# Kernel tuning notes

Hardware: AMD Instinct MI355X
Metric: run time of the kernel (lower is better)

The kernel has to match this reference:

```python
import jax, jax.numpy as jnp
import numpy as np

B, S, D = 1024, 200, 128
NQ, NC, NQD, NCD = 50000, 1000, 101, 101


def _linear_params(k, fan_in, fan_out):
    bound = 1.0 / np.sqrt(fan_in)
    kw, kb = jax.random.split(k)
    W = jax.random.uniform(kw, (fan_out, fan_in), minval=-bound, maxval=bound, dtype=jnp.float32)
    b = jax.random.uniform(kb, (fan_out,), minval=-bound, maxval=bound, dtype=jnp.float32)
    return W, b


def setup_inputs() -> dict:
    key = jax.random.key(0)
    ks = jax.random.split(key, 17)
    Wx, bx = _linear_params(ks[0], 4 * D, D)
    Ws1, bs1 = _linear_params(ks[1], D, D)
    Ws2, bs2 = _linear_params(ks[2], D, D)
    Wp1, bp1 = _linear_params(ks[3], 2 * D, D)
    Wp2, bp2 = _linear_params(ks[4], 2 * D, D)
    Wk, bk = _linear_params(ks[5], 4 * D, D)
    Eq = jax.random.normal(ks[6], (NQ, D), dtype=jnp.float32)
    Ec = jax.random.normal(ks[7], (NC, D), dtype=jnp.float32)
    Eqd = jax.random.normal(ks[8], (NQD, D), dtype=jnp.float32)
    Ecd = jax.random.normal(ks[9], (NCD, D), dtype=jnp.float32)
    Ecorr = jax.random.normal(ks[10], (2, D), dtype=jnp.float32)
    # xavier_uniform init for h_pre (torch: gain*sqrt(6/(fan_in+fan_out)) on [B,D])
    bh = np.sqrt(6.0 / (B + D))
    h0 = jax.random.uniform(ks[11], (B, D), minval=-bh, maxval=bh, dtype=jnp.float32)
    question_seq = jax.random.randint(ks[12], (B, S), 0, NQ)
    concept_seq = jax.random.randint(ks[13], (B, S), 0, NC)
    question_diff_seq = jax.random.randint(ks[14], (B, S), 0, NQD)
    concept_diff_seq = jax.random.randint(ks[15], (B, S), 0, NCD)
    correct_seq = jax.random.randint(ks[16], (B, S), 0, 2)
    return dict(question_seq=question_seq, concept_seq=concept_seq,
                question_diff_seq=question_diff_seq, concept_diff_seq=concept_diff_seq,
                correct_seq=correct_seq,
                Eq=Eq, Ec=Ec, Eqd=Eqd, Ecd=Ecd, Ecorr=Ecorr,
                Wx=Wx, bx=bx, Ws1=Ws1, bs1=bs1, Ws2=Ws2, bs2=bs2,
                Wp1=Wp1, bp1=bp1, Wp2=Wp2, bp2=bp2, Wk=Wk, bk=bk, h0=h0)


def reference(question_seq, concept_seq, question_diff_seq, concept_diff_seq, correct_seq,
              Eq, Ec, Eqd, Ecd, Ecorr,
              Wx, bx, Ws1, bs1, Ws2, bs2, Wp1, bp1, Wp2, bp2, Wk, bk, h0):
    qe = Eq[question_seq]            # [B,S,D]
    ce = Ec[concept_seq]
    qde = Eqd[question_diff_seq]
    cde = Ecd[concept_diff_seq]
    corr = Ecorr[correct_seq]
    # generate_x_MLP applied to all timesteps at once (same math as per-step)
    x = jnp.concatenate([qe, ce, qde, cde], axis=-1) @ Wx.T + bx  # [B,S,D]
    # time-major inputs for the scan over t = 0 .. S-2
    xs = (jnp.swapaxes(x[:, :-1], 0, 1),      # x_t       [S-1,B,D]
          jnp.swapaxes(x[:, 1:], 0, 1),       # x_{t+1}
          jnp.swapaxes(corr[:, :-1], 0, 1),
          jnp.swapaxes(qde[:, :-1], 0, 1),
          jnp.swapaxes(cde[:, :-1], 0, 1))

    def step(h_pre, inp):
        xt, xnext, ct, qdt, cdt = inp
        s_in = xt - h_pre
        sdf = jax.nn.sigmoid(s_in @ Ws1.T + bs1) * jnp.tanh(s_in @ Ws2.T + bs2)  # dropout=eval identity
        p_in = jnp.concatenate([sdf, ct], axis=-1)
        pka = jax.nn.sigmoid(p_in @ Wp1.T + bp1) * jnp.tanh(p_in @ Wp2.T + bp2)
        k_in = jnp.concatenate([h_pre, ct, qdt, cdt], axis=-1)
        g = jax.nn.sigmoid(k_in @ Wk.T + bk)
        h = g * h_pre + (1.0 - g) * pka
        yt = jax.nn.sigmoid(jnp.sum(xnext * h, axis=-1))  # [B]
        return h, yt

    _, ys = jax.lax.scan(step, h0, xs)  # ys: [S-1,B]
    y = jnp.concatenate([ys.T, jnp.zeros((question_seq.shape[0], 1), x.dtype)], axis=1)  # [B,S], y[:, S-1]=0
    return y
```

## Files before the change

### kernel.cpp

```cpp
#include <hip/hip_runtime.h>


#define S_LEN 200
#define NBATCH 1024
#define DIM 128
#define LOG2E 1.4426950408889634f

typedef short short8 __attribute__((ext_vector_type(8)));
typedef float f32x4 __attribute__((ext_vector_type(4)));

__device__ __forceinline__ unsigned short f2b(float f) {
  union { float f; unsigned u; } v; v.f = f;
  unsigned r = (v.u + 0x7FFFu + ((v.u >> 16) & 1u)) >> 16;
  return (unsigned short)r;
}
__device__ __forceinline__ float b2f(unsigned short b) {
  union { unsigned u; float f; } v; v.u = ((unsigned)b) << 16;
  return v.f;
}
__device__ __forceinline__ float fast_sigmoid(float x) {
  return __builtin_amdgcn_rcpf(1.0f + __builtin_amdgcn_exp2f(-LOG2E * x));
}
__device__ __forceinline__ float fast_tanh(float x) {
  return 2.0f * __builtin_amdgcn_rcpf(1.0f + __builtin_amdgcn_exp2f(-2.0f * LOG2E * x)) - 1.0f;
}
__device__ __forceinline__ void wg_barrier_lds() {
  __asm__ volatile("s_waitcnt lgkmcnt(0)\n\ts_barrier" ::: "memory");
}

__global__ void proj_all_kernel(const float* __restrict__ Eq, const float* __restrict__ Ec,
                                const float* __restrict__ Eqd, const float* __restrict__ Ecd,
                                const float* __restrict__ Ecorr,
                                const float* __restrict__ Wx,
                                const float* __restrict__ Wp1, const float* __restrict__ bp1,
                                const float* __restrict__ Wp2, const float* __restrict__ bp2,
                                const float* __restrict__ Wk, const float* __restrict__ bk,
                                unsigned short* __restrict__ Tq, unsigned short* __restrict__ Tc,
                                unsigned short* __restrict__ Tqd, unsigned short* __restrict__ Tcd,
                                unsigned short* __restrict__ Tkqd, unsigned short* __restrict__ Tkcd,
                                float* __restrict__ Tkc, float* __restrict__ Tp1c,
                                float* __restrict__ Tp2c) {
  const int bid = blockIdx.x;
  const int tid = threadIdx.x;
  if (bid >= 3202) {
    const int blk = bid - 3202;
    if (blk < 101) {
      const int o = tid & 127, half = tid >> 7;
      const float* e = (half ? Ecd : Eqd) + (size_t)blk * DIM;
      const float* wr = Wk + (size_t)o * 512 + (half ? 384 : 256);
      float a = 0.f;
      for (int k = 0; k < DIM; ++k) a = fmaf(e[k], wr[k], a);
      (half ? Tkcd : Tkqd)[blk * DIM + o] = f2b(a);
    } else {
      for (int idx = tid; idx < 768; idx += 256) {
        const int t = idx >> 8, e = (idx >> 7) & 1, o = idx & 127;
        const float* ec = Ecorr + e * DIM;
        const float* wr; float bias; float* dst;
        if (t == 0)      { wr = Wp1 + (size_t)o * 256 + 128; bias = bp1[o]; dst = Tp1c; }
        else if (t == 1) { wr = Wp2 + (size_t)o * 256 + 128; bias = bp2[o]; dst = Tp2c; }
        else             { wr = Wk  + (size_t)o * 512 + 128; bias = bk[o];  dst = Tkc;  }
        float a = bias;
        for (int k = 0; k < DIM; ++k) a = fmaf(ec[k], wr[k], a);
        dst[e * DIM + o] = a;
      }
    }
    return;
  }
  const float* E; int M, coff, r0; unsigned short* T;
  if (bid < 3125)      { E = Eq;  M = 50000; coff = 0;   T = Tq;  r0 = bid * 16; }
  else if (bid < 3188) { E = Ec;  M = 1000;  coff = 128; T = Tc;  r0 = (bid - 3125) * 16; }
  else if (bid < 3195) { E = Eqd; M = 101;   coff = 256; T = Tqd; r0 = (bid - 3188) * 16; }
  else                 { E = Ecd; M = 101;   coff = 384; T = Tcd; r0 = (bid - 3195) * 16; }

  __shared__ __align__(16) unsigned short A[16][136];
  {
    const int row = tid >> 4, c8 = (tid & 15) * 8;
    union U8 { uint4 v; unsigned short s[8]; } o;
    if (r0 + row < M) {
      const float4 e0 = *(const float4*)(E + (size_t)(r0 + row) * DIM + c8);
      const float4 e1 = *(const float4*)(E + (size_t)(r0 + row) * DIM + c8 + 4);
      o.s[0] = f2b(e0.x); o.s[1] = f2b(e0.y); o.s[2] = f2b(e0.z); o.s[3] = f2b(e0.w);
      o.s[4] = f2b(e1.x); o.s[5] = f2b(e1.y); o.s[6] = f2b(e1.z); o.s[7] = f2b(e1.w);
    } else {
      o.v = make_uint4(0, 0, 0, 0);
    }
    *(uint4*)&A[row][c8] = o.v;
  }
  __syncthreads();
  const int w = tid >> 6, L = tid & 63, q = L >> 4, m = L & 15;
  short8 bf[2][4];
#pragma unroll
  for (int T2 = 0; T2 < 2; ++T2) {
    const int n = 32 * w + 16 * T2 + m;
#pragma unroll
    for (int kb = 0; kb < 4; ++kb) {
      const float* src = Wx + (size_t)n * 512 + coff + kb * 32 + q * 8;
      const float4 v0 = *(const float4*)src;
      const float4 v1 = *(const float4*)(src + 4);
      short8 f;
      f[0] = (short)f2b(v0.x); f[1] = (short)f2b(v0.y);
      f[2] = (short)f2b(v0.z); f[3] = (short)f2b(v0.w);
      f[4] = (short)f2b(v1.x); f[5] = (short)f2b(v1.y);
      f[6] = (short)f2b(v1.z); f[7] = (short)f2b(v1.w);
      bf[T2][kb] = f;
    }
  }
  short8 af[4];
#pragma unroll
  for (int kb = 0; kb < 4; ++kb) af[kb] = *(const short8*)&A[m][kb * 32 + q * 8];
  const f32x4 vzero = {0.f, 0.f, 0.f, 0.f};
  f32x4 acc[2] = {vzero, vzero};
#pragma unroll
  for (int kb = 0; kb < 4; ++kb) {
#pragma unroll
    for (int T2 = 0; T2 < 2; ++T2)
      acc[T2] = __builtin_amdgcn_mfma_f32_16x16x32_bf16(af[kb], bf[T2][kb], acc[T2], 0, 0, 0);
  }
#pragma unroll
  for (int T2 = 0; T2 < 2; ++T2) {
    const int col = 32 * w + 16 * T2 + m;
#pragma unroll
    for (int i = 0; i < 4; ++i) {
      const int r = r0 + q * 4 + i;
      if (r < M) T[(size_t)r * DIM + col] = f2b(acc[T2][i]);
    }
  }
}

__global__ void build_x_kernel(const int* __restrict__ qs, const int* __restrict__ cs,
                               const int* __restrict__ qds, const int* __restrict__ cds,
                               const unsigned short* __restrict__ Tq, const unsigned short* __restrict__ Tc,
                               const unsigned short* __restrict__ Tqd, const unsigned short* __restrict__ Tcd,
                               const float* __restrict__ bx, unsigned short* __restrict__ xg,
                               float* __restrict__ SSg) {
  const int r = blockIdx.x * 16 + (threadIdx.x >> 4);
  const int c8 = (threadIdx.x & 15) * 8;
  const int s = r >> 10, b = r & 1023;
  const int q = qs[b * S_LEN + s], c = cs[b * S_LEN + s];
  const int qd = qds[b * S_LEN + s], cd = cds[b * S_LEN + s];
  union U8 { uint4 v; unsigned short s[8]; };
  U8 vq, vc, vd, ve, o;
  vq.v = *(const uint4*)(Tq + (size_t)q * DIM + c8);
  vc.v = *(const uint4*)(Tc + (size_t)c * DIM + c8);
  vd.v = *(const uint4*)(Tqd + (size_t)qd * DIM + c8);
  ve.v = *(const uint4*)(Tcd + (size_t)cd * DIM + c8);
  const float4 bx0 = *(const float4*)(bx + c8);
  const float4 bx1 = *(const float4*)(bx + c8 + 4);
  float bb[8] = {bx0.x, bx0.y, bx0.z, bx0.w, bx1.x, bx1.y, bx1.z, bx1.w};
  float part = 0.f;
#pragma unroll
  for (int j = 0; j < 8; ++j) {
    const float sv = b2f(vq.s[j]) + b2f(vc.s[j]) + b2f(vd.s[j]) + b2f(ve.s[j]) + bb[j];
    o.s[j] = f2b(sv);
    const float xr = b2f(o.s[j]);
    part = fmaf(xr, xr, part);
  }
  *(uint4*)(xg + (size_t)r * DIM + c8) = o.v;
#pragma unroll
  for (int off = 1; off <= 8; off <<= 1) part += __shfl_xor(part, off, 64);
  if ((threadIdx.x & 15) == 0) SSg[r] = part;
}

__global__ void gemm_xwk_kernel(const unsigned short* __restrict__ xg,
                                const float* __restrict__ Wk,
                                unsigned short* __restrict__ GG) {
  const int tid = threadIdx.x;
  const int w = tid >> 6, L = tid & 63, q = L >> 4, m = L & 15;
  const int rbase = blockIdx.x * 64;
  short8 wk[2][4];
#pragma unroll
  for (int T = 0; T < 2; ++T) {
    const int n = 32 * w + 16 * T + m;
#pragma unroll
    for (int kb = 0; kb < 4; ++kb) {
      const float* src = Wk + (size_t)n * 512 + kb * 32 + q * 8;
      const float4 v0 = *(const float4*)src;
      const float4 v1 = *(const float4*)(src + 4);
      short8 f;
      f[0] = (short)f2b(v0.x); f[1] = (short)f2b(v0.y);
      f[2] = (short)f2b(v0.z); f[3] = (short)f2b(v0.w);
      f[4] = (short)f2b(v1.x); f[5] = (short)f2b(v1.y);
      f[6] = (short)f2b(v1.z); f[7] = (short)f2b(v1.w);
      wk[T][kb] = f;
    }
  }
  const f32x4 vzero = {0.f, 0.f, 0.f, 0.f};
#pragma unroll
  for (int mt = 0; mt < 4; ++mt) {
    short8 af[4];
#pragma unroll
    for (int kb = 0; kb < 4; ++kb)
      af[kb] = *(const short8*)(xg + (size_t)(rbase + mt * 16 + m) * DIM + kb * 32 + q * 8);
    f32x4 acc[2] = {vzero, vzero};
#pragma unroll
    for (int kb = 0; kb < 4; ++kb) {
#pragma unroll
      for (int T = 0; T < 2; ++T)
        acc[T] = __builtin_amdgcn_mfma_f32_16x16x32_bf16(af[kb], wk[T][kb], acc[T], 0, 0, 0);
    }
#pragma unroll
    for (int T = 0; T < 2; ++T) {
      const int col = 32 * w + 16 * T + m;
#pragma unroll
      for (int i = 0; i < 4; ++i)
        GG[(size_t)(rbase + mt * 16 + q * 4 + i) * DIM + col] = f2b(acc[T][i]);
    }
  }
}

__global__ void build_gpre_add_kernel(const int* __restrict__ corr, const int* __restrict__ qds,
                                      const int* __restrict__ cds,
                                      const float* __restrict__ Tkc,
                                      const unsigned short* __restrict__ Tkqd,
                                      const unsigned short* __restrict__ Tkcd,
                                      unsigned short* __restrict__ gg) {
  const int r = blockIdx.x * 16 + (threadIdx.x >> 4);
  const int c8 = (threadIdx.x & 15) * 8;
  const int t = r >> 10, b = r & 1023;
  const int ci = corr[b * S_LEN + t], qi = qds[b * S_LEN + t], di = cds[b * S_LEN + t];
  union U8 { uint4 v; unsigned short s[8]; };
  U8 vq, vc, vg, o;
  vg.v = *(const uint4*)(gg + (size_t)r * DIM + c8);
  vq.v = *(const uint4*)(Tkqd + (size_t)qi * DIM + c8);
  vc.v = *(const uint4*)(Tkcd + (size_t)di * DIM + c8);
  const float4 k0 = *(const float4*)(Tkc + (size_t)ci * DIM + c8);
  const float4 k1 = *(const float4*)(Tkc + (size_t)ci * DIM + c8 + 4);
  float kk[8] = {k0.x, k0.y, k0.z, k0.w, k1.x, k1.y, k1.z, k1.w};
#pragma unroll
  for (int j = 0; j < 8; ++j)
    o.s[j] = f2b(b2f(vg.s[j]) + kk[j] + b2f(vq.s[j]) + b2f(vc.s[j]));
  *(uint4*)(gg + (size_t)r * DIM + c8) = o.v;
}

__global__ __launch_bounds__(512, 2) void scan_kernel(
    const unsigned short* __restrict__ xg,
    const unsigned short* __restrict__ gg,
    const float* __restrict__ SSg,
    const float* __restrict__ h0,
    const float* __restrict__ Ws1, const float* __restrict__ bs1,
    const float* __restrict__ Ws2, const float* __restrict__ bs2,
    const float* __restrict__ Wp1, const float* __restrict__ Wp2,
    const float* __restrict__ Wk,
    const float* __restrict__ gTp1c, const float* __restrict__ gTp2c,
    const int* __restrict__ corr_seq,
    float* __restrict__ outp) {
  __shared__ __align__(16) unsigned short Sbuf[16][136];
  __shared__ __align__(16) unsigned short Pbuf[16][136];

  const int tid = threadIdx.x;
  const int w = tid >> 6, L = tid & 63, q = L >> 4, m = L & 15;
  const int col16 = 16 * w + m;
  const int rbase = blockIdx.x << 4;

  short8 wf[5][4];
  {
    const float* Wptr[5] = {Ws1, Ws2, Wp1, Wp2, Wk};
    const int ldw[5] = {128, 128, 256, 256, 512};
#pragma unroll
    for (int M = 0; M < 5; ++M) {
#pragma unroll
      for (int kb = 0; kb < 4; ++kb) {
        const float* src = Wptr[M] + (size_t)col16 * ldw[M] + kb * 32 + q * 8;
        const float4 v0 = *(const float4*)src;
        const float4 v1 = *(const float4*)(src + 4);
        short8 f;
        f[0] = (short)f2b(v0.x); f[1] = (short)f2b(v0.y);
        f[2] = (short)f2b(v0.z); f[3] = (short)f2b(v0.w);
        f[4] = (short)f2b(v1.x); f[5] = (short)f2b(v1.y);
        f[6] = (short)f2b(v1.z); f[7] = (short)f2b(v1.w);
        wf[M][kb] = f;
      }
    }
  }
  const float bs1v = bs1[col16], bs2v = bs2[col16];
  const float tp1v0 = gTp1c[col16], tp1v1 = gTp1c[DIM + col16];
  const float tp2v0 = gTp2c[col16], tp2v1 = gTp2c[DIM + col16];

  float h[4];
#pragma unroll
  for (int i = 0; i < 4; ++i) {
    const int b = rbase + q * 4 + i;
    const float hv = h0[(size_t)b * DIM + col16];
    h[i] = hv;
    const float xt = b2f(xg[(size_t)b * DIM + col16]);
    Sbuf[q * 4 + i][col16] = f2b(xt - hv);
  }
  if (tid < 16) outp[(size_t)(rbase + tid) * S_LEN + (S_LEN - 1)] = 0.0f;

  unsigned short xpA[4], ggA[4], xpB[4], ggB[4];
  int cpA[4], cpB[4];
  short8 xfA[4], xfB[4];
  float ssA, ssB;
#pragma unroll
  for (int i = 0; i < 4; ++i) {
    const int b = rbase + q * 4 + i;
    xpA[i] = xg[((size_t)1 * NBATCH + b) * DIM + col16];
    ggA[i] = gg[((size_t)0 * NBATCH + b) * DIM + col16];
    cpA[i] = corr_seq[b * S_LEN + 0];
    xpB[i] = xg[((size_t)2 * NBATCH + b) * DIM + col16];
    ggB[i] = gg[((size_t)1 * NBATCH + b) * DIM + col16];
    cpB[i] = corr_seq[b * S_LEN + 1];
  }
#pragma unroll
  for (int kb = 0; kb < 4; ++kb) {
    xfA[kb] = *(const short8*)(xg + ((size_t)0 * NBATCH + rbase + m) * DIM + kb * 32 + q * 8);
    xfB[kb] = *(const short8*)(xg + ((size_t)1 * NBATCH + rbase + m) * DIM + kb * 32 + q * 8);
  }
  ssA = SSg[(size_t)0 * NBATCH + rbase + m];
  ssB = SSg[(size_t)1 * NBATCH + rbase + m];

  const f32x4 vzero = {0.f, 0.f, 0.f, 0.f};

#define STEP(TCUR, XP, GP, CP, XF, SSP)                                        \
  do {                                                                         \
    const int t_ = (TCUR);                                                     \
    float xnv[4], ggv[4];                                                      \
    int cin[4];                                                                \
    short8 xfr[4];                                                             \
    float ssv = SSP;                                                           \
    _Pragma("unroll") for (int i = 0; i < 4; ++i) {                            \
      xnv[i] = b2f(XP[i]);                                                     \
      ggv[i] = b2f(GP[i]);                                                     \
      cin[i] = CP[i];                                                          \
    }                                                                          \
    _Pragma("unroll") for (int kb = 0; kb < 4; ++kb) xfr[kb] = XF[kb];         \
    {                                                                          \
      const int tp_ = (t_ + 2 <= 198) ? t_ + 2 : 198;                          \
      _Pragma("unroll") for (int i = 0; i < 4; ++i) {                          \
        const int b = rbase + q * 4 + i;                                       \
        XP[i] = xg[((size_t)(tp_ + 1) * NBATCH + b) * DIM + col16];            \
        GP[i] = gg[((size_t)tp_ * NBATCH + b) * DIM + col16];                  \
        CP[i] = corr_seq[b * S_LEN + tp_];                                     \
      }                                                                        \
      _Pragma("unroll") for (int kb = 0; kb < 4; ++kb)                         \
        XF[kb] = *(const short8*)(xg + ((size_t)tp_ * NBATCH + rbase + m) * DIM + kb * 32 + q * 8); \
      SSP = SSg[(size_t)tp_ * NBATCH + rbase + m];                             \
    }                                                                          \
    wg_barrier_lds();                                       \
    short8 sf[4];                                                              \
    _Pragma("unroll") for (int kb = 0; kb < 4; ++kb)                           \
        sf[kb] = *(const short8*)&Sbuf[m][kb * 32 + q * 8];                    \
    f32x4 a1 = vzero, a2 = vzero, c1 = vzero, dt = vzero;                      \
    _Pragma("unroll") for (int kb = 0; kb < 4; ++kb) {                         \
      a1 = __builtin_amdgcn_mfma_f32_16x16x32_bf16(sf[kb], wf[0][kb], a1, 0, 0, 0); \
      a2 = __builtin_amdgcn_mfma_f32_16x16x32_bf16(sf[kb], wf[1][kb], a2, 0, 0, 0); \
      c1 = __builtin_amdgcn_mfma_f32_16x16x32_bf16(sf[kb], wf[4][kb], c1, 0, 0, 0); \
      dt = __builtin_amdgcn_mfma_f32_16x16x32_bf16(sf[kb], xfr[kb], dt, 0, 0, 0);   \
    }                                                                          \
    if (t_ > 0 && w == 0 && q == (m >> 2)) {                                   \
      const int ii = m & 3;                                                    \
      const float D = ii == 0 ? dt[0] : ii == 1 ? dt[1] : ii == 2 ? dt[2] : dt[3]; \
      outp[(size_t)(rbase + m) * S_LEN + (t_ - 1)] = fast_sigmoid(ssv - D);    \
    }                                                                          \
    _Pragma("unroll") for (int i = 0; i < 4; ++i) {                            \
      const float sg = fast_sigmoid(a1[i] + bs1v);                             \
      const float th = fast_tanh(a2[i] + bs2v);                                \
      Pbuf[q * 4 + i][col16] = f2b(sg * th);                                   \
    }                                                                          \
    wg_barrier_lds();                                          \
    short8 pf[4];                                                              \
    _Pragma("unroll") for (int kb = 0; kb < 4; ++kb)                           \
        pf[kb] = *(const short8*)&Pbuf[m][kb * 32 + q * 8];                    \
    f32x4 p1 = vzero, p2 = vzero;                                              \
    _Pragma("unroll") for (int kb = 0; kb < 4; ++kb) {                         \
      p1 = __builtin_amdgcn_mfma_f32_16x16x32_bf16(pf[kb], wf[2][kb], p1, 0, 0, 0); \
      p2 = __builtin_amdgcn_mfma_f32_16x16x32_bf16(pf[kb], wf[3][kb], p2, 0, 0, 0); \
    }                                                                          \
    _Pragma("unroll") for (int i = 0; i < 4; ++i) {                            \
      const float g = fast_sigmoid(ggv[i] - c1[i]);                            \
      const float t1 = cin[i] ? tp1v1 : tp1v0;                                 \
      const float t2 = cin[i] ? tp2v1 : tp2v0;                                 \
      const float pka = fast_sigmoid(p1[i] + t1) * fast_tanh(p2[i] + t2);      \
      const float hn = pka + g * (h[i] - pka);                                 \
      h[i] = hn;                                                               \
      Sbuf[q * 4 + i][col16] = f2b(xnv[i] - hn);                               \
    }                                                                          \
  } while (0)

  for (int t2 = 0; t2 < 198; t2 += 2) {
    STEP(t2, xpA, ggA, cpA, xfA, ssA);
    STEP(t2 + 1, xpB, ggB, cpB, xfB, ssB);
  }
  STEP(198, xpA, ggA, cpA, xfA, ssA);
#undef STEP

  wg_barrier_lds();
  {
    short8 sf[4], xf9[4];
#pragma unroll
    for (int kb = 0; kb < 4; ++kb) {
      sf[kb] = *(const short8*)&Sbuf[m][kb * 32 + q * 8];
      xf9[kb] = *(const short8*)(xg + ((size_t)199 * NBATCH + rbase + m) * DIM + kb * 32 + q * 8);
    }
    f32x4 dt = vzero;
#pragma unroll
    for (int kb = 0; kb < 4; ++kb)
      dt = __builtin_amdgcn_mfma_f32_16x16x32_bf16(sf[kb], xf9[kb], dt, 0, 0, 0);
    const float ssv = SSg[(size_t)199 * NBATCH + rbase + m];
    if (w == 0 && q == (m >> 2)) {
      const int ii = m & 3;
      const float D = ii == 0 ? dt[0] : ii == 1 ? dt[1] : ii == 2 ? dt[2] : dt[3];
      outp[(size_t)(rbase + m) * S_LEN + (S_LEN - 2)] = fast_sigmoid(ssv - D);
    }
  }
}

extern "C" void kernel_launch(void* const* d_in, const int* in_sizes, int n_in,
                              void* d_out, int out_size, void* d_ws, size_t ws_size,
                              hipStream_t stream) {
  const int* qs    = (const int*)d_in[0];
  const int* cs    = (const int*)d_in[1];
  const int* qds   = (const int*)d_in[2];
  const int* cds   = (const int*)d_in[3];
  const int* corr  = (const int*)d_in[4];
  const float* Eq    = (const float*)d_in[5];
  const float* Ec    = (const float*)d_in[6];
  const float* Eqd   = (const float*)d_in[7];
  const float* Ecd   = (const float*)d_in[8];
  const float* Ecorr = (const float*)d_in[9];
  const float* Wx  = (const float*)d_in[10];
  const float* bx  = (const float*)d_in[11];
  const float* Ws1 = (const float*)d_in[12];
  const float* bs1 = (const float*)d_in[13];
  const float* Ws2 = (const float*)d_in[14];
  const float* bs2 = (const float*)d_in[15];
  const float* Wp1 = (const float*)d_in[16];
  const float* bp1 = (const float*)d_in[17];
  const float* Wp2 = (const float*)d_in[18];
  const float* bp2 = (const float*)d_in[19];
  const float* Wk  = (const float*)d_in[20];
  const float* bk  = (const float*)d_in[21];
  const float* h0  = (const float*)d_in[22];

  char* ws = (char*)d_ws;
  const size_t xbytes = (size_t)S_LEN * NBATCH * DIM * 2;
  const size_t A = (xbytes + 255) & ~(size_t)255;
  const size_t ggbytes = (size_t)(S_LEN - 1) * NBATCH * DIM * 2;
  unsigned short* X  = (unsigned short*)ws;
  unsigned short* GG = (unsigned short*)(ws + A);
  unsigned short* Tq  = GG;
  unsigned short* Tc  = (unsigned short*)(ws + A + (size_t)50000 * DIM * 2);
  unsigned short* Tqd = (unsigned short*)(ws + A + (size_t)51000 * DIM * 2);
  unsigned short* Tcd = (unsigned short*)(ws + A + (size_t)51101 * DIM * 2);
  size_t off = A + ((ggbytes + 255) & ~(size_t)255);
  auto alloc = [&](size_t bytes) {
    void* p = ws + off;
    off = (off + bytes + 255) & ~(size_t)255;
    return p;
  };
  unsigned short* Tkqd = (unsigned short*)alloc((size_t)101 * DIM * 2);
  unsigned short* Tkcd = (unsigned short*)alloc((size_t)101 * DIM * 2);
  float* Tkc  = (float*)alloc((size_t)2 * DIM * 4);
  float* Tp1c = (float*)alloc((size_t)2 * DIM * 4);
  float* Tp2c = (float*)alloc((size_t)2 * DIM * 4);
  float* SS   = (float*)alloc((size_t)S_LEN * NBATCH * 4);

  proj_all_kernel<<<3304, 256, 0, stream>>>(Eq, Ec, Eqd, Ecd, Ecorr, Wx,
                                            Wp1, bp1, Wp2, bp2, Wk, bk,
                                            Tq, Tc, Tqd, Tcd, Tkqd, Tkcd, Tkc, Tp1c, Tp2c);
  build_x_kernel<<<(S_LEN * NBATCH) / 16, 256, 0, stream>>>(qs, cs, qds, cds, Tq, Tc, Tqd, Tcd,
                                                            bx, X, SS);
  gemm_xwk_kernel<<<((S_LEN - 1) * NBATCH) / 64, 256, 0, stream>>>(X, Wk, GG);
  build_gpre_add_kernel<<<((S_LEN - 1) * NBATCH) / 16, 256, 0, stream>>>(corr, qds, cds, Tkc, Tkqd, Tkcd, GG);
  scan_kernel<<<64, 512, 0, stream>>>(X, GG, SS, h0, Ws1, bs1, Ws2, bs2, Wp1, Wp2, Wk,
                                      Tp1c, Tp2c, corr, (float*)d_out);
}
```

Measured before the change: 556.0 us.

## Fuse gate-bias gather into Wk GEMM, enlarge projection tiles, trim scan step work

The separate build_gpre_add pass is folded into the Wk GEMM epilogue. Its gathered bias rows are staged in LDS and added before the bf16 store, which removes one full read-modify-write over GG. The embedding projection kernel now handles 64 rows per block instead of 16, reusing the converted Wx fragments across four M-tiles. The scan kernel reads correctness as precomputed floats with linear blending, uses pointer-increment prefetch, restricts the output dot-product MFMA and its loads to wave 0, and packs bf16 conversions in pairs. The costs are an extra corrf buffer and more LDS in the GEMM.

```diff
diff --git a/kernel.cpp b/kernel.cpp
--- a/kernel.cpp
+++ b/kernel.cpp
@@ -1,4 +1,5 @@
 #include <hip/hip_runtime.h>
+#include <hip/hip_bf16.h>
 
 
 #define S_LEN 200
@@ -17,6 +18,11 @@
 __device__ __forceinline__ float b2f(unsigned short b) {
   union { unsigned u; float f; } v; v.u = ((unsigned)b) << 16;
   return v.f;
+}
+__device__ __forceinline__ unsigned pk_bf16(float lo, float hi) {
+  __hip_bfloat162 t = __float22bfloat162_rn(make_float2(lo, hi));
+  union { __hip_bfloat162 h; unsigned u; } cv; cv.h = t;
+  return cv.u;
 }
 __device__ __forceinline__ float fast_sigmoid(float x) {
   return __builtin_amdgcn_rcpf(1.0f + __builtin_amdgcn_exp2f(-LOG2E * x));
@@ -42,8 +48,8 @@
                                 float* __restrict__ Tp2c) {
   const int bid = blockIdx.x;
   const int tid = threadIdx.x;
-  if (bid >= 3202) {
-    const int blk = bid - 3202;
+  if (bid >= 802) {
+    const int blk = bid - 802;
     if (blk < 101) {
       const int o = tid & 127, half = tid >> 7;
       const float* e = (half ? Ecd : Eqd) + (size_t)blk * DIM;
@@ -67,24 +73,28 @@
     return;
   }
   const float* E; int M, coff, r0; unsigned short* T;
-  if (bid < 3125)      { E = Eq;  M = 50000; coff = 0;   T = Tq;  r0 = bid * 16; }
-  else if (bid < 3188) { E = Ec;  M = 1000;  coff = 128; T = Tc;  r0 = (bid - 3125) * 16; }
-  else if (bid < 3195) { E = Eqd; M = 101;   coff = 256; T = Tqd; r0 = (bid - 3188) * 16; }
-  else                 { E = Ecd; M = 101;   coff = 384; T = Tcd; r0 = (bid - 3195) * 16; }
-
-  __shared__ __align__(16) unsigned short A[16][136];
+  if (bid < 782)      { E = Eq;  M = 50000; coff = 0;   T = Tq;  r0 = bid * 64; }
+  else if (bid < 798) { E = Ec;  M = 1000;  coff = 128; T = Tc;  r0 = (bid - 782) * 64; }
+  else if (bid < 800) { E = Eqd; M = 101;   coff = 256; T = Tqd; r0 = (bid - 798) * 64; }
+  else                { E = Ecd; M = 101;   coff = 384; T = Tcd; r0 = (bid - 800) * 64; }
+
+  __shared__ __align__(16) unsigned short A[64][136];
   {
-    const int row = tid >> 4, c8 = (tid & 15) * 8;
+    const int row = tid >> 2, cb = (tid & 3) * 32;
     union U8 { uint4 v; unsigned short s[8]; } o;
-    if (r0 + row < M) {
-      const float4 e0 = *(const float4*)(E + (size_t)(r0 + row) * DIM + c8);
-      const float4 e1 = *(const float4*)(E + (size_t)(r0 + row) * DIM + c8 + 4);
-      o.s[0] = f2b(e0.x); o.s[1] = f2b(e0.y); o.s[2] = f2b(e0.z); o.s[3] = f2b(e0.w);
-      o.s[4] = f2b(e1.x); o.s[5] = f2b(e1.y); o.s[6] = f2b(e1.z); o.s[7] = f2b(e1.w);
-    } else {
-      o.v = make_uint4(0, 0, 0, 0);
-    }
-    *(uint4*)&A[row][c8] = o.v;
+#pragma unroll
+    for (int cc = 0; cc < 4; ++cc) {
+      const int c8 = cb + cc * 8;
+      if (r0 + row < M) {
+        const float4 e0 = *(const float4*)(E + (size_t)(r0 + row) * DIM + c8);
+        const float4 e1 = *(const float4*)(E + (size_t)(r0 + row) * DIM + c8 + 4);
+        o.s[0] = f2b(e0.x); o.s[1] = f2b(e0.y); o.s[2] = f2b(e0.z); o.s[3] = f2b(e0.w);
+        o.s[4] = f2b(e1.x); o.s[5] = f2b(e1.y); o.s[6] = f2b(e1.z); o.s[7] = f2b(e1.w);
+      } else {
+        o.v = make_uint4(0, 0, 0, 0);
+      }
+      *(uint4*)&A[row][c8] = o.v;
+    }
   }
   __syncthreads();
   const int w = tid >> 6, L = tid & 63, q = L >> 4, m = L & 15;
@@ -105,34 +115,38 @@
       bf[T2][kb] = f;
     }
   }
-  short8 af[4];
-#pragma unroll
-  for (int kb = 0; kb < 4; ++kb) af[kb] = *(const short8*)&A[m][kb * 32 + q * 8];
   const f32x4 vzero = {0.f, 0.f, 0.f, 0.f};
-  f32x4 acc[2] = {vzero, vzero};
-#pragma unroll
-  for (int kb = 0; kb < 4; ++kb) {
-#pragma unroll
-    for (int T2 = 0; T2 < 2; ++T2)
-      acc[T2] = __builtin_amdgcn_mfma_f32_16x16x32_bf16(af[kb], bf[T2][kb], acc[T2], 0, 0, 0);
-  }
-#pragma unroll
-  for (int T2 = 0; T2 < 2; ++T2) {
-    const int col = 32 * w + 16 * T2 + m;
-#pragma unroll
-    for (int i = 0; i < 4; ++i) {
-      const int r = r0 + q * 4 + i;
-      if (r < M) T[(size_t)r * DIM + col] = f2b(acc[T2][i]);
+#pragma unroll
+  for (int mt = 0; mt < 4; ++mt) {
+    short8 af[4];
+#pragma unroll
+    for (int kb = 0; kb < 4; ++kb) af[kb] = *(const short8*)&A[mt * 16 + m][kb * 32 + q * 8];
+    f32x4 acc[2] = {vzero, vzero};
+#pragma unroll
+    for (int kb = 0; kb < 4; ++kb) {
+#pragma unroll
+      for (int T2 = 0; T2 < 2; ++T2)
+        acc[T2] = __builtin_amdgcn_mfma_f32_16x16x32_bf16(af[kb], bf[T2][kb], acc[T2], 0, 0, 0);
+    }
+#pragma unroll
+    for (int T2 = 0; T2 < 2; ++T2) {
+      const int col = 32 * w + 16 * T2 + m;
+#pragma unroll
+      for (int i = 0; i < 4; ++i) {
+        const int r = r0 + mt * 16 + q * 4 + i;
+        if (r < M) T[(size_t)r * DIM + col] = f2b(acc[T2][i]);
+      }
     }
   }
 }
 
 __global__ void build_x_kernel(const int* __restrict__ qs, const int* __restrict__ cs,
                                const int* __restrict__ qds, const int* __restrict__ cds,
+                               const int* __restrict__ corr,
                                const unsigned short* __restrict__ Tq, const unsigned short* __restrict__ Tc,
                                const unsigned short* __restrict__ Tqd, const unsigned short* __restrict__ Tcd,
                                const float* __restrict__ bx, unsigned short* __restrict__ xg,
-                               float* __restrict__ SSg) {
+                               float* __restrict__ SSg, float* __restrict__ corrf) {
   const int r = blockIdx.x * 16 + (threadIdx.x >> 4);
   const int c8 = (threadIdx.x & 15) * 8;
   const int s = r >> 10, b = r & 1023;
@@ -158,15 +172,44 @@
   *(uint4*)(xg + (size_t)r * DIM + c8) = o.v;
 #pragma unroll
   for (int off = 1; off <= 8; off <<= 1) part += __shfl_xor(part, off, 64);
-  if ((threadIdx.x & 15) == 0) SSg[r] = part;
-}
-
-__global__ void gemm_xwk_kernel(const unsigned short* __restrict__ xg,
-                                const float* __restrict__ Wk,
-                                unsigned short* __restrict__ GG) {
+  if ((threadIdx.x & 15) == 0) {
+    SSg[r] = part;
+    corrf[r] = (float)corr[b * S_LEN + s];
+  }
+}
+
+__global__ void gemm_xg_kernel(const unsigned short* __restrict__ xg,
+                               const float* __restrict__ Wk,
+                               const int* __restrict__ corr, const int* __restrict__ qds,
+                               const int* __restrict__ cds,
+                               const float* __restrict__ Tkc,
+                               const unsigned short* __restrict__ Tkqd,
+                               const unsigned short* __restrict__ Tkcd,
+                               unsigned short* __restrict__ GG) {
   const int tid = threadIdx.x;
+  const int r0 = blockIdx.x * 64;
+  __shared__ __align__(16) unsigned short TS[64][136];
+  {
+    const int row = tid >> 2, cb = (tid & 3) * 32;
+    const int r = r0 + row, t = r >> 10, b = r & 1023;
+    const int ci = corr[b * S_LEN + t], qi = qds[b * S_LEN + t], di = cds[b * S_LEN + t];
+    union U8 { uint4 v; unsigned short s[8]; };
+#pragma unroll
+    for (int cc = 0; cc < 4; ++cc) {
+      const int c8 = cb + cc * 8;
+      U8 vq, vc, o;
+      vq.v = *(const uint4*)(Tkqd + (size_t)qi * DIM + c8);
+      vc.v = *(const uint4*)(Tkcd + (size_t)di * DIM + c8);
+      const float4 k0 = *(const float4*)(Tkc + (size_t)ci * DIM + c8);
+      const float4 k1 = *(const float4*)(Tkc + (size_t)ci * DIM + c8 + 4);
+      float kk[8] = {k0.x, k0.y, k0.z, k0.w, k1.x, k1.y, k1.z, k1.w};
+#pragma unroll
+      for (int j = 0; j < 8; ++j) o.s[j] = f2b(kk[j] + b2f(vq.s[j]) + b2f(vc.s[j]));
+      *(uint4*)&TS[row][c8] = o.v;
+    }
+  }
+  __syncthreads();
   const int w = tid >> 6, L = tid & 63, q = L >> 4, m = L & 15;
-  const int rbase = blockIdx.x * 64;
   short8 wk[2][4];
 #pragma unroll
   for (int T = 0; T < 2; ++T) {
@@ -190,7 +233,7 @@
     short8 af[4];
 #pragma unroll
     for (int kb = 0; kb < 4; ++kb)
-      af[kb] = *(const short8*)(xg + (size_t)(rbase + mt * 16 + m) * DIM + kb * 32 + q * 8);
+      af[kb] = *(const short8*)(xg + (size_t)(r0 + mt * 16 + m) * DIM + kb * 32 + q * 8);
     f32x4 acc[2] = {vzero, vzero};
 #pragma unroll
     for (int kb = 0; kb < 4; ++kb) {
@@ -202,47 +245,25 @@
     for (int T = 0; T < 2; ++T) {
       const int col = 32 * w + 16 * T + m;
 #pragma unroll
-      for (int i = 0; i < 4; ++i)
-        GG[(size_t)(rbase + mt * 16 + q * 4 + i) * DIM + col] = f2b(acc[T][i]);
-    }
-  }
-}
-
-__global__ void build_gpre_add_kernel(const int* __restrict__ corr, const int* __restrict__ qds,
-                                      const int* __restrict__ cds,
-                                      const float* __restrict__ Tkc,
-                                      const unsigned short* __restrict__ Tkqd,
-                                      const unsigned short* __restrict__ Tkcd,
-                                      unsigned short* __restrict__ gg) {
-  const int r = blockIdx.x * 16 + (threadIdx.x >> 4);
-  const int c8 = (threadIdx.x & 15) * 8;
-  const int t = r >> 10, b = r & 1023;
-  const int ci = corr[b * S_LEN + t], qi = qds[b * S_LEN + t], di = cds[b * S_LEN + t];
-  union U8 { uint4 v; unsigned short s[8]; };
-  U8 vq, vc, vg, o;
-  vg.v = *(const uint4*)(gg + (size_t)r * DIM + c8);
-  vq.v = *(const uint4*)(Tkqd + (size_t)qi * DIM + c8);
-  vc.v = *(const uint4*)(Tkcd + (size_t)di * DIM + c8);
-  const float4 k0 = *(const float4*)(Tkc + (size_t)ci * DIM + c8);
-  const float4 k1 = *(const float4*)(Tkc + (size_t)ci * DIM + c8 + 4);
-  float kk[8] = {k0.x, k0.y, k0.z, k0.w, k1.x, k1.y, k1.z, k1.w};
-#pragma unroll
-  for (int j = 0; j < 8; ++j)
-    o.s[j] = f2b(b2f(vg.s[j]) + kk[j] + b2f(vq.s[j]) + b2f(vc.s[j]));
-  *(uint4*)(gg + (size_t)r * DIM + c8) = o.v;
+      for (int i = 0; i < 4; ++i) {
+        const int row64 = mt * 16 + q * 4 + i;
+        GG[(size_t)(r0 + row64) * DIM + col] = f2b(acc[T][i] + b2f(TS[row64][col]));
+      }
+    }
+  }
 }
 
 __global__ __launch_bounds__(512, 2) void scan_kernel(
     const unsigned short* __restrict__ xg,
     const unsigned short* __restrict__ gg,
     const float* __restrict__ SSg,
+    const float* __restrict__ corrf,
     const float* __restrict__ h0,
     const float* __restrict__ Ws1, const float* __restrict__ bs1,
     const float* __restrict__ Ws2, const float* __restrict__ bs2,
     const float* __restrict__ Wp1, const float* __restrict__ Wp2,
     const float* __restrict__ Wk,
     const float* __restrict__ gTp1c, const float* __restrict__ gTp2c,
-    const int* __restrict__ corr_seq,
     float* __restrict__ outp) {
   __shared__ __align__(16) unsigned short Sbuf[16][136];
   __shared__ __align__(16) unsigned short Pbuf[16][136];
@@ -251,6 +272,7 @@
   const int w = tid >> 6, L = tid & 63, q = L >> 4, m = L & 15;
   const int col16 = 16 * w + m;
   const int rbase = blockIdx.x << 4;
+  const size_t SB = (size_t)NBATCH * DIM;
 
   short8 wf[5][4];
   {
@@ -273,8 +295,8 @@
     }
   }
   const float bs1v = bs1[col16], bs2v = bs2[col16];
-  const float tp1v0 = gTp1c[col16], tp1v1 = gTp1c[DIM + col16];
-  const float tp2v0 = gTp2c[col16], tp2v1 = gTp2c[DIM + col16];
+  const float tp1v0 = gTp1c[col16], dtp1 = gTp1c[DIM + col16] - tp1v0;
+  const float tp2v0 = gTp2c[col16], dtp2 = gTp2c[DIM + col16] - tp2v0;
 
   float h[4];
 #pragma unroll
@@ -286,76 +308,90 @@
     Sbuf[q * 4 + i][col16] = f2b(xt - hv);
   }
   if (tid < 16) outp[(size_t)(rbase + tid) * S_LEN + (S_LEN - 1)] = 0.0f;
-
-  unsigned short xpA[4], ggA[4], xpB[4], ggB[4];
-  int cpA[4], cpB[4];
-  short8 xfA[4], xfB[4];
-  float ssA, ssB;
+  float* poy = outp + (size_t)(rbase + m) * S_LEN;
+
+  unsigned short XPA[4], XPB[4], GPA[4], GPB[4];
+  float4 CFA, CFB;
+  short8 XFA[4], XFB[4];
+  float SSA, SSB;
+  const unsigned short* pxA = xg + 3 * SB + (size_t)(rbase + q * 4) * DIM + col16;
+  const unsigned short* pxB = pxA + SB;
+  const unsigned short* pgA = gg + 2 * SB + (size_t)(rbase + q * 4) * DIM + col16;
+  const unsigned short* pgB = pgA + SB;
+  const float* pcA = corrf + 2 * NBATCH + rbase + q * 4;
+  const float* pcB = pcA + NBATCH;
+  const unsigned short* pfA = xg + 2 * SB + (size_t)(rbase + m) * DIM + q * 8;
+  const unsigned short* pfB = pfA + SB;
+  const float* psA = SSg + 2 * NBATCH + rbase + m;
+  const float* psB = psA + NBATCH;
 #pragma unroll
   for (int i = 0; i < 4; ++i) {
-    const int b = rbase + q * 4 + i;
-    xpA[i] = xg[((size_t)1 * NBATCH + b) * DIM + col16];
-    ggA[i] = gg[((size_t)0 * NBATCH + b) * DIM + col16];
-    cpA[i] = corr_seq[b * S_LEN + 0];
-    xpB[i] = xg[((size_t)2 * NBATCH + b) * DIM + col16];
-    ggB[i] = gg[((size_t)1 * NBATCH + b) * DIM + col16];
-    cpB[i] = corr_seq[b * S_LEN + 1];
-  }
+    XPA[i] = xg[SB + (size_t)(rbase + q * 4 + i) * DIM + col16];
+    XPB[i] = xg[2 * SB + (size_t)(rbase + q * 4 + i) * DIM + col16];
+    GPA[i] = gg[(size_t)(rbase + q * 4 + i) * DIM + col16];
+    GPB[i] = gg[SB + (size_t)(rbase + q * 4 + i) * DIM + col16];
+  }
+  CFA = *(const float4*)(corrf + rbase + q * 4);
+  CFB = *(const float4*)(corrf + NBATCH + rbase + q * 4);
 #pragma unroll
   for (int kb = 0; kb < 4; ++kb) {
-    xfA[kb] = *(const short8*)(xg + ((size_t)0 * NBATCH + rbase + m) * DIM + kb * 32 + q * 8);
-    xfB[kb] = *(const short8*)(xg + ((size_t)1 * NBATCH + rbase + m) * DIM + kb * 32 + q * 8);
-  }
-  ssA = SSg[(size_t)0 * NBATCH + rbase + m];
-  ssB = SSg[(size_t)1 * NBATCH + rbase + m];
+    XFA[kb] = *(const short8*)(xg + (size_t)(rbase + m) * DIM + kb * 32 + q * 8);
+    XFB[kb] = *(const short8*)(xg + SB + (size_t)(rbase + m) * DIM + kb * 32 + q * 8);
+  }
+  SSA = SSg[rbase + m];
+  SSB = SSg[NBATCH + rbase + m];
 
   const f32x4 vzero = {0.f, 0.f, 0.f, 0.f};
 
-#define STEP(TCUR, XP, GP, CP, XF, SSP)                                        \
+#define STEP(TCUR, XP, GP, CF, PX, PG, PC, XF, SSR, PF, PS)                    \
   do {                                                                         \
     const int t_ = (TCUR);                                                     \
-    float xnv[4], ggv[4];                                                      \
-    int cin[4];                                                                \
-    short8 xfr[4];                                                             \
-    float ssv = SSP;                                                           \
+    float xnv[4], ggv[4], cfv[4];                                              \
     _Pragma("unroll") for (int i = 0; i < 4; ++i) {                            \
-      xnv[i] = b2f(XP[i]);                                                     \
-      ggv[i] = b2f(GP[i]);                                                     \
-      cin[i] = CP[i];                                                          \
-    }                                                                          \
-    _Pragma("unroll") for (int kb = 0; kb < 4; ++kb) xfr[kb] = XF[kb];         \
-    {                                                                          \
-      const int tp_ = (t_ + 2 <= 198) ? t_ + 2 : 198;                          \
-      _Pragma("unroll") for (int i = 0; i < 4; ++i) {                          \
-        const int b = rbase + q * 4 + i;                                       \
-        XP[i] = xg[((size_t)(tp_ + 1) * NBATCH + b) * DIM + col16];            \
-        GP[i] = gg[((size_t)tp_ * NBATCH + b) * DIM + col16];                  \
-        CP[i] = corr_seq[b * S_LEN + tp_];                                     \
-      }                                                                        \
+      xnv[i] = b2f(XP[i]); ggv[i] = b2f(GP[i]);                                \
+    }                                                                          \
+    cfv[0] = CF.x; cfv[1] = CF.y; cfv[2] = CF.z; cfv[3] = CF.w;                \
+    short8 xfr[4]; float ssv = SSR;                                            \
+    if (w == 0) {                                                              \
+      _Pragma("unroll") for (int kb = 0; kb < 4; ++kb) xfr[kb] = XF[kb];       \
+    }                                                                          \
+    _Pragma("unroll") for (int i = 0; i < 4; ++i) {                            \
+      XP[i] = PX[i * DIM]; GP[i] = PG[i * DIM];                                \
+    }                                                                          \
+    CF = *(const float4*)PC;                                                   \
+    PX += 2 * SB; PG += 2 * SB; PC += 2 * NBATCH;                              \
+    if (w == 0) {                                                              \
       _Pragma("unroll") for (int kb = 0; kb < 4; ++kb)                         \
-        XF[kb] = *(const short8*)(xg + ((size_t)tp_ * NBATCH + rbase + m) * DIM + kb * 32 + q * 8); \
-      SSP = SSg[(size_t)tp_ * NBATCH + rbase + m];                             \
+        XF[kb] = *(const short8*)(PF + kb * 32);                               \
+      SSR = *PS;                                                               \
+      PF += 2 * SB; PS += 2 * NBATCH;                                          \
     }                                                                          \
     wg_barrier_lds();                                       \
     short8 sf[4];                                                              \
     _Pragma("unroll") for (int kb = 0; kb < 4; ++kb)                           \
         sf[kb] = *(const short8*)&Sbuf[m][kb * 32 + q * 8];                    \
-    f32x4 a1 = vzero, a2 = vzero, c1 = vzero, dt = vzero;                      \
+    f32x4 a1 = vzero, a2 = vzero, c1 = vzero;                                  \
     _Pragma("unroll") for (int kb = 0; kb < 4; ++kb) {                         \
       a1 = __builtin_amdgcn_mfma_f32_16x16x32_bf16(sf[kb], wf[0][kb], a1, 0, 0, 0); \
       a2 = __builtin_amdgcn_mfma_f32_16x16x32_bf16(sf[kb], wf[1][kb], a2, 0, 0, 0); \
       c1 = __builtin_amdgcn_mfma_f32_16x16x32_bf16(sf[kb], wf[4][kb], c1, 0, 0, 0); \
-      dt = __builtin_amdgcn_mfma_f32_16x16x32_bf16(sf[kb], xfr[kb], dt, 0, 0, 0);   \
-    }                                                                          \
-    if (t_ > 0 && w == 0 && q == (m >> 2)) {                                   \
-      const int ii = m & 3;                                                    \
-      const float D = ii == 0 ? dt[0] : ii == 1 ? dt[1] : ii == 2 ? dt[2] : dt[3]; \
-      outp[(size_t)(rbase + m) * S_LEN + (t_ - 1)] = fast_sigmoid(ssv - D);    \
-    }                                                                          \
-    _Pragma("unroll") for (int i = 0; i < 4; ++i) {                            \
-      const float sg = fast_sigmoid(a1[i] + bs1v);                             \
-      const float th = fast_tanh(a2[i] + bs2v);                                \
-      Pbuf[q * 4 + i][col16] = f2b(sg * th);                                   \
+    }                                                                          \
+    if (w == 0) {                                                              \
+      f32x4 dt = vzero;                                                        \
+      _Pragma("unroll") for (int kb = 0; kb < 4; ++kb)                         \
+        dt = __builtin_amdgcn_mfma_f32_16x16x32_bf16(sf[kb], xfr[kb], dt, 0, 0, 0); \
+      if (t_ > 0 && q == (m >> 2)) {                                           \
+        const int ii = m & 3;                                                  \
+        const float D = ii == 0 ? dt[0] : ii == 1 ? dt[1] : ii == 2 ? dt[2] : dt[3]; \
+        poy[t_ - 1] = fast_sigmoid(ssv - D);                                   \
+      }                                                                        \
+    }                                                                          \
+    _Pragma("unroll") for (int i2 = 0; i2 < 2; ++i2) {                         \
+      const float s0 = fast_sigmoid(a1[2 * i2] + bs1v) * fast_tanh(a2[2 * i2] + bs2v); \
+      const float s1 = fast_sigmoid(a1[2 * i2 + 1] + bs1v) * fast_tanh(a2[2 * i2 + 1] + bs2v); \
+      const unsigned u = pk_bf16(s0, s1);                                      \
+      Pbuf[q * 4 + 2 * i2][col16] = (unsigned short)u;                         \
+      Pbuf[q * 4 + 2 * i2 + 1][col16] = (unsigned short)(u >> 16);             \
     }                                                                          \
     wg_barrier_lds();                                          \
     short8 pf[4];                                                              \
@@ -366,41 +402,43 @@
       p1 = __builtin_amdgcn_mfma_f32_16x16x32_bf16(pf[kb], wf[2][kb], p1, 0, 0, 0); \
       p2 = __builtin_amdgcn_mfma_f32_16x16x32_bf16(pf[kb], wf[3][kb], p2, 0, 0, 0); \
     }                                                                          \
+    float sn[4];                                                               \
     _Pragma("unroll") for (int i = 0; i < 4; ++i) {                            \
       const float g = fast_sigmoid(ggv[i] - c1[i]);                            \
-      const float t1 = cin[i] ? tp1v1 : tp1v0;                                 \
-      const float t2 = cin[i] ? tp2v1 : tp2v0;                                 \
-      const float pka = fast_sigmoid(p1[i] + t1) * fast_tanh(p2[i] + t2);      \
+      const float t1v = fmaf(cfv[i], dtp1, tp1v0);                             \
+      const float t2v = fmaf(cfv[i], dtp2, tp2v0);                             \
+      const float pka = fast_sigmoid(p1[i] + t1v) * fast_tanh(p2[i] + t2v);    \
       const float hn = pka + g * (h[i] - pka);                                 \
       h[i] = hn;                                                               \
-      Sbuf[q * 4 + i][col16] = f2b(xnv[i] - hn);                               \
+      sn[i] = xnv[i] - hn;                                                     \
+    }                                                                          \
+    _Pragma("unroll") for (int i2 = 0; i2 < 2; ++i2) {                         \
+      const unsigned u = pk_bf16(sn[2 * i2], sn[2 * i2 + 1]);                  \
+      Sbuf[q * 4 + 2 * i2][col16] = (unsigned short)u;                         \
+      Sbuf[q * 4 + 2 * i2 + 1][col16] = (unsigned short)(u >> 16);             \
     }                                                                          \
   } while (0)
 
   for (int t2 = 0; t2 < 198; t2 += 2) {
-    STEP(t2, xpA, ggA, cpA, xfA, ssA);
-    STEP(t2 + 1, xpB, ggB, cpB, xfB, ssB);
-  }
-  STEP(198, xpA, ggA, cpA, xfA, ssA);
+    STEP(t2, XPA, GPA, CFA, pxA, pgA, pcA, XFA, SSA, pfA, psA);
+    STEP(t2 + 1, XPB, GPB, CFB, pxB, pgB, pcB, XFB, SSB, pfB, psB);
+  }
+  STEP(198, XPA, GPA, CFA, pxA, pgA, pcA, XFA, SSA, pfA, psA);
 #undef STEP
 
   wg_barrier_lds();
-  {
-    short8 sf[4], xf9[4];
-#pragma unroll
-    for (int kb = 0; kb < 4; ++kb) {
-      sf[kb] = *(const short8*)&Sbuf[m][kb * 32 + q * 8];
-      xf9[kb] = *(const short8*)(xg + ((size_t)199 * NBATCH + rbase + m) * DIM + kb * 32 + q * 8);
-    }
+  if (w == 0) {
+    short8 sf[4];
+#pragma unroll
+    for (int kb = 0; kb < 4; ++kb) sf[kb] = *(const short8*)&Sbuf[m][kb * 32 + q * 8];
     f32x4 dt = vzero;
 #pragma unroll
     for (int kb = 0; kb < 4; ++kb)
-      dt = __builtin_amdgcn_mfma_f32_16x16x32_bf16(sf[kb], xf9[kb], dt, 0, 0, 0);
-    const float ssv = SSg[(size_t)199 * NBATCH + rbase + m];
-    if (w == 0 && q == (m >> 2)) {
+      dt = __builtin_amdgcn_mfma_f32_16x16x32_bf16(sf[kb], XFB[kb], dt, 0, 0, 0);
+    if (q == (m >> 2)) {
       const int ii = m & 3;
       const float D = ii == 0 ? dt[0] : ii == 1 ? dt[1] : ii == 2 ? dt[2] : dt[3];
-      outp[(size_t)(rbase + m) * S_LEN + (S_LEN - 2)] = fast_sigmoid(ssv - D);
+      poy[S_LEN - 2] = fast_sigmoid(SSB - D);
     }
   }
 }
@@ -448,20 +486,21 @@
     off = (off + bytes + 255) & ~(size_t)255;
     return p;
   };
+  float* corrf = (float*)alloc((size_t)S_LEN * NBATCH * 4);
+  float* SS    = (float*)alloc((size_t)S_LEN * NBATCH * 4);
   unsigned short* Tkqd = (unsigned short*)alloc((size_t)101 * DIM * 2);
   unsigned short* Tkcd = (unsigned short*)alloc((size_t)101 * DIM * 2);
   float* Tkc  = (float*)alloc((size_t)2 * DIM * 4);
   float* Tp1c = (float*)alloc((size_t)2 * DIM * 4);
   float* Tp2c = (float*)alloc((size_t)2 * DIM * 4);
-  float* SS   = (float*)alloc((size_t)S_LEN * NBATCH * 4);
-
-  proj_all_kernel<<<3304, 256, 0, stream>>>(Eq, Ec, Eqd, Ecd, Ecorr, Wx,
-                                            Wp1, bp1, Wp2, bp2, Wk, bk,
-                                            Tq, Tc, Tqd, Tcd, Tkqd, Tkcd, Tkc, Tp1c, Tp2c);
-  build_x_kernel<<<(S_LEN * NBATCH) / 16, 256, 0, stream>>>(qs, cs, qds, cds, Tq, Tc, Tqd, Tcd,
-                                                            bx, X, SS);
-  gemm_xwk_kernel<<<((S_LEN - 1) * NBATCH) / 64, 256, 0, stream>>>(X, Wk, GG);
-  build_gpre_add_kernel<<<((S_LEN - 1) * NBATCH) / 16, 256, 0, stream>>>(corr, qds, cds, Tkc, Tkqd, Tkcd, GG);
-  scan_kernel<<<64, 512, 0, stream>>>(X, GG, SS, h0, Ws1, bs1, Ws2, bs2, Wp1, Wp2, Wk,
-                                      Tp1c, Tp2c, corr, (float*)d_out);
-}
+
+  proj_all_kernel<<<904, 256, 0, stream>>>(Eq, Ec, Eqd, Ecd, Ecorr, Wx,
+                                           Wp1, bp1, Wp2, bp2, Wk, bk,
+                                           Tq, Tc, Tqd, Tcd, Tkqd, Tkcd, Tkc, Tp1c, Tp2c);
+  build_x_kernel<<<(S_LEN * NBATCH) / 16, 256, 0, stream>>>(qs, cs, qds, cds, corr,
+                                                            Tq, Tc, Tqd, Tcd, bx, X, SS, corrf);
+  gemm_xg_kernel<<<((S_LEN - 1) * NBATCH) / 64, 256, 0, stream>>>(X, Wk, corr, qds, cds,
+                                                                  Tkc, Tkqd, Tkcd, GG);
+  scan_kernel<<<64, 512, 0, stream>>>(X, GG, SS, corrf, h0, Ws1, bs1, Ws2, bs2,
+                                      Wp1, Wp2, Wk, Tp1c, Tp2c, (float*)d_out);
+}
```

After: 513.7 us. 7.6% less time.
